# Performance work log

Hardware: AMD Instinct MI355X
Metric: run time of the kernel (lower is better)

## Reference

```python
import jax, jax.numpy as jnp
import numpy as np

BATCH = 16384
XD = 64      # x_dim
AD = 16      # a_dim
NC = 8       # number of constraints
PEN = 10.0   # relax_penalty
DELTA = 1.0  # class-K coefficient
ITERS = 250  # FISTA iterations for the dual QP (converges to OSQP solution)


def _cbf_forward(a_des, x, A, B, Qc, cc, dc):
    """Batched CBF-QP safety filter.

    Constraints: g_i(x) = 0.5 x^T Qc_i x + cc_i^T x - dc_i  (g_i <= 0 is safe)
    Barrier:     h_i(x) = -g_i(x),  grad_h = -(Qc_i x + cc_i)
    QP:  min ||a - a_des||^2 + PEN * ||s||^2
         s.t. Lg_h a >= -Lf_h - DELTA*h - s,  s >= 0
    Solved exactly (to FISTA tolerance) via the dual:
         min_{lam>=0} 0.5 lam^T M lam - lam^T q,
    with z = [a; s], H = diag(2*1_AD, 2*PEN*1_NC), z = z0 + H^{-1} G^T lam.
    """
    bsz = a_des.shape[0]
    # constraint values and gradients (the 'autograd jacobian' in the original)
    g_x = 0.5 * jnp.einsum('bi,mij,bj->bm', x, Qc, x) + x @ cc.T - dc[None, :]
    h_x = -g_x                                              # [B, NC]
    grad_h = -(jnp.einsum('mij,bj->bmi', Qc, x) + cc[None])  # [B, NC, XD]
    # Lie derivatives
    Lf_h = jnp.einsum('bmi,bij,bj->bm', grad_h, A, x)        # [B, NC]
    Lg_h = jnp.einsum('bmi,bia->bma', grad_h, B)             # [B, NC, AD]
    bvec = -Lf_h - DELTA * h_x                               # rhs: Lg_h a + s >= bvec

    # dual QP setup: G z >= c, G = [[Lg_h, I],[0, I]], c = [bvec; 0]
    Im = jnp.broadcast_to(jnp.eye(NC, dtype=a_des.dtype), (bsz, NC, NC))
    Gtop = jnp.concatenate([Lg_h, Im], axis=2)                    # [B, NC, AD+NC]
    Gbot = jnp.concatenate([jnp.zeros((bsz, NC, AD), a_des.dtype), Im], axis=2)
    G = jnp.concatenate([Gtop, Gbot], axis=1)                     # [B, 2NC, AD+NC]
    dinv = jnp.concatenate([0.5 * jnp.ones(AD, a_des.dtype),
                            jnp.ones(NC, a_des.dtype) / (2.0 * PEN)])
    Mmat = jnp.einsum('bkn,n,bln->bkl', G, dinv, G)               # [B, 2NC, 2NC]
    q = jnp.concatenate([bvec - jnp.einsum('bma,ba->bm', Lg_h, a_des),
                         jnp.zeros((bsz, NC), a_des.dtype)], axis=1)

    # step size 1/L, L = max eigenvalue of M (not differentiated)
    L = jax.lax.stop_gradient(jnp.linalg.eigvalsh(Mmat)[..., -1]) + 1e-6
    t = (1.0 / L)[:, None]

    lam0 = jnp.zeros((bsz, 2 * NC), a_des.dtype)

    def step(carry, _):
        lam, y, tk = carry
        grad = jnp.einsum('bkl,bl->bk', Mmat, y) - q
        lam_new = jnp.maximum(y - t * grad, 0.0)
        tk1 = 0.5 * (1.0 + jnp.sqrt(1.0 + 4.0 * tk * tk))
        y_new = lam_new + ((tk - 1.0) / tk1) * (lam_new - lam)
        return (lam_new, y_new, tk1), None

    (lam, _, _), _ = jax.lax.scan(step, (lam0, lam0, jnp.float32(1.0)), None, length=ITERS)

    # primal recovery: a = a_des + 0.5 * Lg_h^T lam_top
    a_safe = a_des + 0.5 * jnp.einsum('bma,bm->ba', Lg_h, lam[:, :NC])
    return a_safe


def setup_inputs() -> dict:
    key = jax.random.key(0)
    ks = jax.random.split(key, 7)
    a_des = jax.random.normal(ks[0], (BATCH, AD), jnp.float32)
    x = jax.random.normal(ks[1], (BATCH, XD), jnp.float32)
    A = jax.random.normal(ks[2], (BATCH, XD, XD), jnp.float32) * 0.05
    B = jax.random.normal(ks[3], (BATCH, XD, AD), jnp.float32) * 0.1
    R = jax.random.normal(ks[4], (NC, XD, XD), jnp.float32) * 0.05
    Qc = R + jnp.swapaxes(R, 1, 2)  # symmetric quadratic constraint Hessians
    cc = jax.random.normal(ks[5], (NC, XD), jnp.float32) * 0.1
    dc = jax.random.uniform(ks[6], (NC,), jnp.float32) + 0.5
    return {"a_des": a_des, "x": x, "A": A, "B": B, "Qc": Qc, "cc": cc, "dc": dc}


def reference(a_des, x, A, B, Qc, cc, dc):
    return _cbf_forward(a_des, x, A, B, Qc, cc, dc)
```

## Files before the change

kernel.cpp:

```cpp
#include <hip/hip_runtime.h>
#include <cstddef>

#define NBATCH 16384

struct Betas {
  float b[250];
  static constexpr double csqrt(double x) {
    double g = x > 1.0 ? x : 1.0;
    for (int i = 0; i < 64; ++i) g = 0.5 * (g + x / g);
    return g;
  }
  constexpr Betas() : b{} {
    double tk = 1.0;
    for (int i = 0; i < 250; ++i) {
      double tk1 = 0.5 * (1.0 + csqrt(1.0 + 4.0 * tk * tk));
      b[i] = (float)((tk - 1.0) / tk1);
      tk = tk1;
    }
  }
};
__device__ constexpr Betas BETAS{};

template <int CTRL>
__device__ __forceinline__ float fdpp(float v) {
  return __int_as_float(
      __builtin_amdgcn_mov_dpp(__float_as_int(v), CTRL, 0xF, 0xF, true));
}
__device__ __forceinline__ float rowsum16(float p) {
  p += fdpp<0x121>(p);
  p += fdpp<0x122>(p);
  p += fdpp<0x124>(p);
  p += fdpp<0x128>(p);
  return p;
}

__global__ __launch_bounds__(256) void cbf_k1_gh(
    const float* __restrict__ Qc, const float* __restrict__ cc,
    const float* __restrict__ X, float* __restrict__ gh) {
  __shared__ float tile[64 * 132];
  const int tid = threadIdx.x;
  const int e   = tid & 63;
  const int rc  = tid >> 6;
  const int b0  = (blockIdx.x & 255) * 64;
  const int r0  = (blockIdx.x >> 8) * 256;

  float4 xr[16];
  const float4* xp = (const float4*)(X + (size_t)(b0 + e) * 64);
#pragma unroll
  for (int c = 0; c < 16; ++c) xr[c] = xp[c];

  const int rcu = __builtin_amdgcn_readfirstlane(rc);

  for (int p = 0; p < 2; ++p) {
    const int rbase = r0 + p * 128 + rcu * 32;
    const float* wbase = Qc + (size_t)rbase * 64;
#pragma unroll 4
    for (int rl = 0; rl < 32; ++rl) {
      const float4* w = (const float4*)(wbase + rl * 64);
      float a0 = 0.f, a1 = 0.f;
#pragma unroll
      for (int c = 0; c < 16; ++c) {
        float4 wv = w[c];
        a0 = fmaf(wv.x, xr[c].x, a0);
        a1 = fmaf(wv.y, xr[c].y, a1);
        a0 = fmaf(wv.z, xr[c].z, a0);
        a1 = fmaf(wv.w, xr[c].w, a1);
      }
      tile[e * 132 + rc * 32 + rl] = a0 + a1 + cc[rbase + rl];
    }
    __syncthreads();
    {
      const int c  = tid & 31;
      const int bq = tid >> 5;
#pragma unroll
      for (int bp = 0; bp < 8; ++bp) {
        const int bb = bp * 8 + bq;
        float4 v = *(const float4*)&tile[bb * 132 + c * 4];
        *(float4*)(gh + (size_t)(b0 + bb) * 512 + (r0 + p * 128) + c * 4) = v;
      }
    }
    __syncthreads();
  }
}

#define XOFF  0
#define BVOFF 64
#define BOFF  72
#define GHOFF (72 + 1024)
#define LGOFF (1096 + 544)
#define AXOFF (1640 + 160)
#define ESTR  (1800 + 64)

__global__ __launch_bounds__(256) void cbf_k2_setup(
    const float* __restrict__ X, const float* __restrict__ Abat,
    const float* __restrict__ Bbat, const float* __restrict__ cc,
    const float* __restrict__ dc, const float* __restrict__ a_des,
    const float* __restrict__ gh, float* __restrict__ S_ws,
    float* __restrict__ LgT_ws, float* __restrict__ qu_ws) {
  __shared__ float smem[4 * ESTR];
  const int tid  = threadIdx.x;
  const int sub  = tid >> 6;
  const int lane = tid & 63;
  const int b    = blockIdx.x * 4 + sub;
  float* sm = smem + sub * ESTR;

  const float xi = X[(size_t)b * 64 + lane];
  sm[XOFF + lane] = xi;
  {
    const float4* bp = (const float4*)(Bbat + (size_t)b * 1024);
#pragma unroll
    for (int n = 0; n < 4; ++n) {
      float4 v = bp[n * 64 + lane];
      *(float4*)&sm[BOFF + n * 256 + lane * 4] = v;
    }
  }
  {
    const float4* gp = (const float4*)(gh + (size_t)b * 512);
    float4 g0 = gp[lane];
    float4 g1 = gp[64 + lane];
    const int f0 = lane * 4, f1 = 256 + lane * 4;
    *(float4*)&sm[GHOFF + (f0 >> 6) * 68 + (f0 & 63)] = g0;
    *(float4*)&sm[GHOFF + (f1 >> 6) * 68 + (f1 & 63)] = g1;
  }
  __syncthreads();

  {
    const float4* ap = (const float4*)(Abat + (size_t)b * 4096);
    const int cg = lane & 15;
    const int rg = lane >> 4;
    const float4 xv = *(const float4*)&sm[XOFF + cg * 4];
#pragma unroll
    for (int n = 0; n < 16; ++n) {
      float4 av = ap[n * 64 + lane];
      float p = av.x * xv.x + av.y * xv.y + av.z * xv.z + av.w * xv.w;
      p = rowsum16(p);
      if (cg == 0) sm[AXOFF + n * 4 + rg] = p;
    }
  }
  __syncthreads();

  {
    const int m  = lane >> 3;
    const int ig = lane & 7;
    const float4 ghA = *(const float4*)&sm[GHOFF + m * 68 + ig * 8];
    const float4 ghB = *(const float4*)&sm[GHOFF + m * 68 + ig * 8 + 4];
    const float4 xA  = *(const float4*)&sm[XOFF + ig * 8];
    const float4 xB  = *(const float4*)&sm[XOFF + ig * 8 + 4];
    const float4 axA = *(const float4*)&sm[AXOFF + ig * 8];
    const float4 axB = *(const float4*)&sm[AXOFF + ig * 8 + 4];
    const float4 ccA = *(const float4*)(cc + m * 64 + ig * 8);
    const float4 ccB = *(const float4*)(cc + m * 64 + ig * 8 + 4);
    float p1 = ghA.x * xA.x + ghA.y * xA.y + ghA.z * xA.z + ghA.w * xA.w
             + ghB.x * xB.x + ghB.y * xB.y + ghB.z * xB.z + ghB.w * xB.w;
    float p2 = ghA.x * axA.x + ghA.y * axA.y + ghA.z * axA.z + ghA.w * axA.w
             + ghB.x * axB.x + ghB.y * axB.y + ghB.z * axB.z + ghB.w * axB.w;
    float p3 = ccA.x * xA.x + ccA.y * xA.y + ccA.z * xA.z + ccA.w * xA.w
             + ccB.x * xB.x + ccB.y * xB.y + ccB.z * xB.z + ccB.w * xB.w;
    p1 += __shfl_xor(p1, 1); p1 += __shfl_xor(p1, 2); p1 += __shfl_xor(p1, 4);
    p2 += __shfl_xor(p2, 1); p2 += __shfl_xor(p2, 2); p2 += __shfl_xor(p2, 4);
    p3 += __shfl_xor(p3, 1); p3 += __shfl_xor(p3, 2); p3 += __shfl_xor(p3, 4);
    if (ig == 0) {
      sm[BVOFF + m] = p2 + 0.5f * (p1 + p3) - dc[m];
    }
  }

  const int mq  = lane >> 3;
  const int ap2 = lane & 7;
  {
    float acc0 = 0.f, acc1 = 0.f;
#pragma unroll
    for (int c = 0; c < 16; ++c) {
      float4 gv = *(const float4*)&sm[GHOFF + mq * 68 + 4 * c];
#pragma unroll
      for (int n = 0; n < 4; ++n) {
        float2 bv2 = *(const float2*)&sm[BOFF + (4 * c + n) * 16 + 2 * ap2];
        float gvn = (n == 0) ? gv.x : ((n == 1) ? gv.y : ((n == 2) ? gv.z : gv.w));
        acc0 = fmaf(gvn, bv2.x, acc0);
        acc1 = fmaf(gvn, bv2.y, acc1);
      }
    }
    const float lg0 = -acc0, lg1 = -acc1;
    LgT_ws[(size_t)b * 128 + (2 * ap2) * 8 + mq]     = lg0;
    LgT_ws[(size_t)b * 128 + (2 * ap2 + 1) * 8 + mq] = lg1;
    sm[LGOFF + mq * 20 + 2 * ap2]     = lg0;
    sm[LGOFF + mq * 20 + 2 * ap2 + 1] = lg1;
  }
  __syncthreads();

  const int kq = lane >> 3;
  const int lq = lane & 7;
  {
    float s = 0.f;
#pragma unroll
    for (int c = 0; c < 4; ++c) {
      float4 ka = *(const float4*)&sm[LGOFF + kq * 20 + 4 * c];
      float4 la = *(const float4*)&sm[LGOFF + lq * 20 + 4 * c];
      s = fmaf(ka.x, la.x, s);
      s = fmaf(ka.y, la.y, s);
      s = fmaf(ka.z, la.z, s);
      s = fmaf(ka.w, la.w, s);
    }
    S_ws[(size_t)b * 64 + kq * 8 + lq] = 0.5f * s;
  }

  {
    float2 ad2 = *(const float2*)(a_des + (size_t)b * 16 + 2 * lq);
    float2 kg  = *(const float2*)&sm[LGOFF + kq * 20 + 2 * lq];
    float p = kg.x * ad2.x + kg.y * ad2.y;
    p += __shfl_xor(p, 1);
    p += __shfl_xor(p, 2);
    p += __shfl_xor(p, 4);
    if (lq == 0) qu_ws[(size_t)b * 8 + kq] = sm[BVOFF + kq] - p;
  }
}

__global__ __launch_bounds__(256) void cbf_k3_fista(
    const float* __restrict__ S_ws, const float* __restrict__ qu_ws,
    const float* __restrict__ LgT_ws, const float* __restrict__ a_des,
    float* __restrict__ out) {
  const int gt = blockIdx.x * 256 + threadIdx.x;
  const int e  = gt >> 2;
  const int q  = gt & 3;

  const float4* Sp = (const float4*)(S_ws + (size_t)e * 64);
  const float4 sl0 = Sp[q * 2],       sl1 = Sp[q * 2 + 1];
  const float4 sh0 = Sp[(q + 4) * 2], sh1 = Sp[(q + 4) * 2 + 1];
  const float qu_lo = qu_ws[(size_t)e * 8 + q];
  const float qu_hi = qu_ws[(size_t)e * 8 + q + 4];

#define MV(ylo, yhi, alo, ahi) do {                                          \
    float b0 = fdpp<0x00>(ylo), b1 = fdpp<0x55>(ylo);                        \
    float b2 = fdpp<0xAA>(ylo), b3 = fdpp<0xFF>(ylo);                        \
    float b4 = fdpp<0x00>(yhi), b5 = fdpp<0x55>(yhi);                        \
    float b6 = fdpp<0xAA>(yhi), b7 = fdpp<0xFF>(yhi);                        \
    float t0 = sl0.x * b0, t1 = sl0.y * b1;                                  \
    t0 = fmaf(sl0.z, b2, t0); t1 = fmaf(sl0.w, b3, t1);                      \
    t0 = fmaf(sl1.x, b4, t0); t1 = fmaf(sl1.y, b5, t1);                      \
    t0 = fmaf(sl1.z, b6, t0); t1 = fmaf(sl1.w, b7, t1);                      \
    alo = t0 + t1;                                                           \
    float u0 = sh0.x * b0, u1 = sh0.y * b1;                                  \
    u0 = fmaf(sh0.z, b2, u0); u1 = fmaf(sh0.w, b3, u1);                      \
    u0 = fmaf(sh1.x, b4, u0); u1 = fmaf(sh1.y, b5, u1);                      \
    u0 = fmaf(sh1.z, b6, u0); u1 = fmaf(sh1.w, b7, u1);                      \
    ahi = u0 + u1;                                                           \
  } while (0)

  float vl = 1.f, vh = 1.f, svl, svh;
#pragma unroll 4
  for (int it = 0; it < 40; ++it) {
    MV(vl, vh, svl, svh);
    float am = fmaxf(fabsf(svl), fabsf(svh));
    am = fmaxf(am, fdpp<0xB1>(am));
    am = fmaxf(am, fdpp<0x4E>(am));
    float r = 1.f / fmaxf(am, 1e-30f);
    vl = svl * r; vh = svh * r;
  }
  MV(vl, vh, svl, svh);
  float num = vl * svl + vh * svh;
  float den = vl * vl + vh * vh;
  num += fdpp<0xB1>(num); den += fdpp<0xB1>(den);
  num += fdpp<0x4E>(num); den += fdpp<0x4E>(den);
  float mu = fmaxf((num / fmaxf(den, 1e-30f)) * 1.001f, 0.f);
  const float lmax = 0.5f * ((0.1f + mu) + sqrtf(fmaf(mu, mu, 0.01f)));
  const float t = 1.0f / (lmax + 1e-6f);

  float yul = 0.f, yuh = 0.f, yvl = 0.f, yvh = 0.f;
  float lul = 0.f, luh = 0.f, lvl_ = 0.f, lvh = 0.f;
#pragma unroll 5
  for (int it = 0; it < 250; ++it) {
    const float beta = BETAS.b[it];
    const float wl = 0.05f * (yul + yvl);
    const float wh = 0.05f * (yuh + yvh);
    float al, ah;
    MV(yul, yuh, al, ah);
    const float gul = al + wl - qu_lo;
    const float guh = ah + wh - qu_hi;
    const float lunl = fmaxf(fmaf(-t, gul, yul), 0.f);
    const float lunh = fmaxf(fmaf(-t, guh, yuh), 0.f);
    const float lvnl = fmaxf(fmaf(-t, wl, yvl), 0.f);
    const float lvnh = fmaxf(fmaf(-t, wh, yvh), 0.f);
    yul = fmaf(beta, lunl - lul, lunl); lul = lunl;
    yuh = fmaf(beta, lunh - luh, lunh); luh = lunh;
    yvl = fmaf(beta, lvnl - lvl_, lvnl); lvl_ = lvnl;
    yvh = fmaf(beta, lvnh - lvh, lvnh); lvh = lvnh;
  }
#undef MV

  const float l0 = fdpp<0x00>(lul), l1 = fdpp<0x55>(lul);
  const float l2 = fdpp<0xAA>(lul), l3 = fdpp<0xFF>(lul);
  const float l4 = fdpp<0x00>(luh), l5 = fdpp<0x55>(luh);
  const float l6 = fdpp<0xAA>(luh), l7 = fdpp<0xFF>(luh);
  const float4* Lp = (const float4*)(LgT_ws + (size_t)e * 128 + q * 32);
  const float4 ad  = *(const float4*)(a_des + (size_t)e * 16 + q * 4);
  float o[4];
#pragma unroll
  for (int j = 0; j < 4; ++j) {
    float4 ga = Lp[j * 2], gb = Lp[j * 2 + 1];
    float s = ga.x * l0 + ga.y * l1 + ga.z * l2 + ga.w * l3
            + gb.x * l4 + gb.y * l5 + gb.z * l6 + gb.w * l7;
    o[j] = 0.5f * s;
  }
  float4 ov;
  ov.x = ad.x + o[0]; ov.y = ad.y + o[1];
  ov.z = ad.z + o[2]; ov.w = ad.w + o[3];
  *(float4*)(out + (size_t)e * 16 + q * 4) = ov;
}

extern "C" void kernel_launch(void* const* d_in, const int* in_sizes, int n_in,
                              void* d_out, int out_size, void* d_ws, size_t ws_size,
                              hipStream_t stream) {
  (void)in_sizes; (void)n_in; (void)out_size; (void)ws_size;
  const float* a_des = (const float*)d_in[0];
  const float* x     = (const float*)d_in[1];
  const float* A     = (const float*)d_in[2];
  const float* B     = (const float*)d_in[3];
  const float* Qc    = (const float*)d_in[4];
  const float* cc    = (const float*)d_in[5];
  const float* dc    = (const float*)d_in[6];
  float* out = (float*)d_out;

  float* gh  = (float*)d_ws;
  float* S   = gh  + (size_t)NBATCH * 512;
  float* LgT = S   + (size_t)NBATCH * 64;
  float* qu  = LgT + (size_t)NBATCH * 128;

  hipLaunchKernelGGL(cbf_k1_gh, dim3(512), dim3(256), 0, stream, Qc, cc, x, gh);
  hipLaunchKernelGGL(cbf_k2_setup, dim3(4096), dim3(256), 0, stream,
                     x, A, B, cc, dc, a_des, gh, S, LgT, qu);
  hipLaunchKernelGGL(cbf_k3_fista, dim3(256), dim3(256), 0, stream,
                     S, qu, LgT, a_des, out);
}
```

Baseline: 524.2 us.

## Stage Qc rows in LDS and write gh directly from registers in k1

The first kernel now copies a 128-row slice of Qc and cc into shared memory once per block, then reads weights from LDS instead of global memory. The shared transpose tile and its two barriers per pass are removed, and each thread stores float4 outputs straight to gh. The grid doubles to 1024 blocks, each covering half as many rows. The risk is less coalesced stores, since each thread writes its own row, plus the extra LDS footprint and staging cost.

```diff
diff --git a/kernel.cpp b/kernel.cpp
--- a/kernel.cpp
+++ b/kernel.cpp
@@ -37,26 +37,40 @@
 __global__ __launch_bounds__(256) void cbf_k1_gh(
     const float* __restrict__ Qc, const float* __restrict__ cc,
     const float* __restrict__ X, float* __restrict__ gh) {
-  __shared__ float tile[64 * 132];
+  __shared__ float qt[128 * 64];
+  __shared__ float cct[128];
   const int tid = threadIdx.x;
   const int e   = tid & 63;
   const int rc  = tid >> 6;
   const int b0  = (blockIdx.x & 255) * 64;
-  const int r0  = (blockIdx.x >> 8) * 256;
+  const int r0  = (blockIdx.x >> 8) * 128;
+
+  {
+    const float4* qsrc = (const float4*)(Qc + (size_t)r0 * 64);
+    float4* qdst = (float4*)qt;
+#pragma unroll
+    for (int i = 0; i < 8; ++i) qdst[i * 256 + tid] = qsrc[i * 256 + tid];
+    if (tid < 32) ((float4*)cct)[tid] = ((const float4*)(cc + r0))[tid];
+  }
 
   float4 xr[16];
-  const float4* xp = (const float4*)(X + (size_t)(b0 + e) * 64);
-#pragma unroll
-  for (int c = 0; c < 16; ++c) xr[c] = xp[c];
+  {
+    const float4* xp = (const float4*)(X + (size_t)(b0 + e) * 64);
+#pragma unroll
+    for (int c = 0; c < 16; ++c) xr[c] = xp[c];
+  }
+  __syncthreads();
 
   const int rcu = __builtin_amdgcn_readfirstlane(rc);
-
-  for (int p = 0; p < 2; ++p) {
-    const int rbase = r0 + p * 128 + rcu * 32;
-    const float* wbase = Qc + (size_t)rbase * 64;
-#pragma unroll 4
-    for (int rl = 0; rl < 32; ++rl) {
-      const float4* w = (const float4*)(wbase + rl * 64);
+  const float* qrow = qt + rcu * 32 * 64;
+  float* ob = gh + (size_t)(b0 + e) * 512 + r0 + rcu * 32;
+
+#pragma unroll 2
+  for (int rg = 0; rg < 8; ++rg) {
+    float o[4];
+#pragma unroll
+    for (int j = 0; j < 4; ++j) {
+      const float4* w = (const float4*)(qrow + (rg * 4 + j) * 64);
       float a0 = 0.f, a1 = 0.f;
 #pragma unroll
       for (int c = 0; c < 16; ++c) {
@@ -66,20 +80,9 @@
         a0 = fmaf(wv.z, xr[c].z, a0);
         a1 = fmaf(wv.w, xr[c].w, a1);
       }
-      tile[e * 132 + rc * 32 + rl] = a0 + a1 + cc[rbase + rl];
-    }
-    __syncthreads();
-    {
-      const int c  = tid & 31;
-      const int bq = tid >> 5;
-#pragma unroll
-      for (int bp = 0; bp < 8; ++bp) {
-        const int bb = bp * 8 + bq;
-        float4 v = *(const float4*)&tile[bb * 132 + c * 4];
-        *(float4*)(gh + (size_t)(b0 + bb) * 512 + (r0 + p * 128) + c * 4) = v;
-      }
-    }
-    __syncthreads();
+      o[j] = a0 + a1 + cct[rcu * 32 + rg * 4 + j];
+    }
+    *(float4*)(ob + rg * 4) = *(const float4*)o;
   }
 }
 
@@ -324,7 +327,7 @@
   float* LgT = S   + (size_t)NBATCH * 64;
   float* qu  = LgT + (size_t)NBATCH * 128;
 
-  hipLaunchKernelGGL(cbf_k1_gh, dim3(512), dim3(256), 0, stream, Qc, cc, x, gh);
+  hipLaunchKernelGGL(cbf_k1_gh, dim3(1024), dim3(256), 0, stream, Qc, cc, x, gh);
   hipLaunchKernelGGL(cbf_k2_setup, dim3(4096), dim3(256), 0, stream,
                      x, A, B, cc, dc, a_des, gh, S, LgT, qu);
   hipLaunchKernelGGL(cbf_k3_fista, dim3(256), dim3(256), 0, stream,
```

Result: faster. 477.1 us (-9.0%).
